# Kernel optimization log

Measured on AMD Instinct MI355X. Metric: run time of the kernel, lower is better.

Reference implementation:

```python
import jax, jax.numpy as jnp
import numpy as np

B, N, EMB = 64, 2048, 128
K1 = 3
L = EMB - K1 + 1            # 126, width after conv1/conv2
K2 = L // 2 + 1             # 64, conv3 kernel width -> conv3 out width = K2 - 1 = 63


def _conv_relu(x, w, b):
    # x: [M, 1, H, W]; w: [O, 1, kh, kw]; VALID conv + bias + relu
    y = jax.lax.conv_general_dilated(
        x, w, window_strides=(1, 1), padding='VALID',
        dimension_numbers=('NCHW', 'OIHW', 'NCHW'))
    return jax.nn.relu(y + b[None, :, None, None])


def _score(pairs, W1, b1, W2, b2, W3, b3, fw1, fb1, fw2, fb2, fw3, fb3):
    # pairs: [M, 2, D] -> score [M]
    x = pairs[:, None]                                  # [M,1,2,D]
    c1 = _conv_relu(x, W1, b1)                          # [M,1,2,L]
    c2 = _conv_relu(x, W2, b2)                          # [M,1,1,L]
    c = jnp.concatenate([c1, c2], axis=2)               # [M,1,3,L]
    c3 = _conv_relu(c, W3, b3)                          # [M,1,1,K2-1]
    h = c3.reshape(c3.shape[0], -1)                     # [M,K2-1]
    h = h @ fw1.T + fb1                                 # [M,K2//4]
    h = h @ fw2.T + fb2                                 # [M,16]
    h = h @ fw3.T + fb3                                 # [M,1]
    return h[:, 0]


def setup_inputs() -> dict:
    key = jax.random.key(0)
    ks = jax.random.split(key, 12)
    users = jax.random.normal(ks[0], (B, N, EMB), jnp.float32)
    top_user = jax.random.normal(ks[1], (B, EMB), jnp.float32)
    question = jax.random.normal(ks[2], (B, EMB), jnp.float32)
    # ragged valid-lengths: uids nonzero for first `len` entries, zero after
    lengths = jax.random.randint(ks[3], (B,), 1, N + 1)
    vals = jax.random.randint(ks[4], (B, N), 1, 10000)
    uids = jnp.where(jnp.arange(N)[None, :] < lengths[:, None], vals, 0).astype(jnp.int64)
    s = 0.1
    return {
        'users': users, 'top_user': top_user, 'question': question, 'uids': uids,
        'W1': jax.random.normal(ks[5], (1, 1, 1, K1), jnp.float32) * s,
        'b1': jnp.zeros((1,), jnp.float32),
        'W2': jax.random.normal(ks[6], (1, 1, 2, K1), jnp.float32) * s,
        'b2': jnp.zeros((1,), jnp.float32),
        'W3': jax.random.normal(ks[7], (1, 1, 3, K2), jnp.float32) * s,
        'b3': jnp.zeros((1,), jnp.float32),
        'fw1': jax.random.normal(ks[8], (K2 // 4, K2 - 1), jnp.float32) * s,
        'fb1': jnp.zeros((K2 // 4,), jnp.float32),
        'fw2': jax.random.normal(ks[9], (16, K2 // 4), jnp.float32) * s,
        'fb2': jnp.zeros((16,), jnp.float32),
        'fw3': jax.random.normal(ks[10], (1, 16), jnp.float32) * s,
        'fb3': jnp.zeros((1,), jnp.float32),
    }


def reference(users, top_user, question, uids,
              W1, b1, W2, b2, W3, b3, fw1, fb1, fw2, fb2, fw3, fb3):
    b, n, d = users.shape
    params = (W1, b1, W2, b2, W3, b3, fw1, fb1, fw2, fb2, fw3, fb3)
    # low-rank pairs: (candidate user, question) for every candidate slot
    q = jnp.broadcast_to(question[:, None], (b, n, d))
    low = jnp.stack([users, q], axis=2).reshape(b * n, 2, d)      # [B*N,2,D]
    high = jnp.stack([top_user, question], axis=1)                # [B,2,D]
    low_s = _score(low, *params).reshape(b, n)                    # [B,N]
    high_s = _score(high, *params)                                # [B]
    # ragged length = index of first zero uid (torch loop breaks there)
    is_zero = uids == 0
    cnt = jnp.where(jnp.any(is_zero, axis=1), jnp.argmax(is_zero, axis=1), n)
    mask = (jnp.arange(n)[None, :] < cnt[:, None]).astype(low_s.dtype)
    return jnp.sum(jax.nn.sigmoid(low_s - high_s[:, None]) * mask)
```

## Files before the change

### kernel.cpp

```cpp
#include <hip/hip_runtime.h>
#include <hip/hip_bf16.h>

typedef __attribute__((ext_vector_type(8))) short short8v;
typedef __attribute__((ext_vector_type(4))) float float4v;

#define NB 64
#define NN 2048
#define ED 128
#define GRID_P 512

#define WS_WEFF  0
#define WS_BEFF  64
#define WS_SHIGH 128
#define WS_QTERM 192
#define WS_QPRE  (192+4096)
#define WS_BPACK (192+4096+8192)
#define WS_QCNT  (WS_BPACK+8192)

static __device__ __forceinline__ unsigned int packbf2(float a, float b) {
    __hip_bfloat162 h = __float22bfloat162_rn(make_float2(a, b));
    return *(unsigned int*)&h;
}

__global__ __launch_bounds__(64) void k_prep(
    const float* __restrict__ top_user, const float* __restrict__ question,
    const float* __restrict__ W1, const float* __restrict__ b1,
    const float* __restrict__ W2, const float* __restrict__ b2,
    const float* __restrict__ W3, const float* __restrict__ b3,
    const float* __restrict__ fw1, const float* __restrict__ fb1,
    const float* __restrict__ fw2, const float* __restrict__ fb2,
    const float* __restrict__ fw3, const float* __restrict__ fb3,
    const int* __restrict__ uids,
    float* __restrict__ ws, float* __restrict__ out)
{
    const int lane = threadIdx.x;
    const int blk = blockIdx.x;

    int act = 0;
    if (blk < NB && lane < 32) act = (uids[blk*NN + lane*64] != 0) ? 1 : 0;

    __shared__ float g[16];
    __shared__ float w3s[192];
    w3s[lane] = W3[lane];
    w3s[64 + lane] = W3[64 + lane];
    w3s[128 + lane] = W3[128 + lane];
    if (lane < 16) {
        float s = 0.f;
        #pragma unroll
        for (int i = 0; i < 16; ++i) s += fw3[i] * fw2[i*16 + lane];
        g[lane] = s;
    }
    __syncthreads();

    if (blk >= NB) {
        const int kt = blk - NB;
        if (kt == 0) {
            if (lane == 0) out[0] = 0.f;
            float wv = 0.f;
            if (lane < 63) {
                #pragma unroll
                for (int k = 0; k < 16; ++k) wv += g[k] * fw1[k*63 + lane];
            }
            ws[WS_WEFF + lane] = wv;
            if (lane == 0) {
                float be = fb3[0];
                #pragma unroll
                for (int i = 0; i < 16; ++i) be += fw3[i] * fb2[i];
                #pragma unroll
                for (int k = 0; k < 16; ++k) be += g[k] * fb1[k];
                ws[WS_BEFF] = be;
            }
        }
        __hip_bfloat16* bp = (__hip_bfloat16*)(ws + WS_BPACK);
        const int g8 = (lane >> 4) * 8, li = lane & 15;
        #pragma unroll
        for (int nt = 0; nt < 4; ++nt) {
            const int tt = nt*16 + li;
            #pragma unroll
            for (int idx = 0; idx < 8; ++idx) {
                const int k = kt*32 + g8 + idx;
                const int j = k - tt;
                const int k2 = k - 128, j2 = k2 - tt;
                const bool v0 = (tt < 63) && (k < 126) && (j >= 0) && (j < 64);
                const bool v2 = (tt < 63) && (k2 >= 0) && (k2 < 126) && (j2 >= 0) && (j2 < 64);
                float v = (v0 ? w3s[j & 63] : 0.f) + (v2 ? w3s[128 + (j2 & 63)] : 0.f);
                bp[((kt*4 + nt)*64 + lane)*8 + idx] = __float2bfloat16(v);
            }
        }
        return;
    }

    {
        const unsigned long long bm = __ballot(act);
        if (lane == 0) ((int*)(ws + WS_QCNT))[blk] = (int)__popcll(bm);
    }

    float wv = 0.f;
    if (lane < 63) {
        #pragma unroll
        for (int k = 0; k < 16; ++k) wv += g[k] * fw1[k*63 + lane];
    }
    float be = fb3[0];
    #pragma unroll
    for (int i = 0; i < 16; ++i) be += fw3[i] * fb2[i];
    #pragma unroll
    for (int k = 0; k < 16; ++k) be += g[k] * fb1[k];

    __shared__ float q[132], tu[132], c1q[128], qt[64];
    __shared__ float4 D4[64];
    const int b = blk;
    ((float2*)q)[lane]  = ((const float2*)(question + b*ED))[lane];
    ((float2*)tu)[lane] = ((const float2*)(top_user + b*ED))[lane];
    if (lane == 63) {
        q[128]=0.f; q[129]=0.f; q[130]=0.f; q[131]=0.f;
        tu[128]=0.f; tu[129]=0.f; tu[130]=0.f; tu[131]=0.f;
    }
    __syncthreads();
    const float w10=W1[0], w11=W1[1], w12=W1[2];
    const float w20=W2[0], w21=W2[1], w22=W2[2];
    const float w23=W2[3], w24=W2[4], w25=W2[5];
    const float b1v=b1[0], b2v=b2[0], b3v=b3[0];
    const int i = 2*lane;
    float c1qa = fmaxf(b1v + w10*q[i]   + w11*q[i+1] + w12*q[i+2], 0.f);
    float c1qb = fmaxf(b1v + w10*q[i+1] + w11*q[i+2] + w12*q[i+3], 0.f);
    float qpa  = w23*q[i]   + w24*q[i+1] + w25*q[i+2];
    float qpb  = w23*q[i+1] + w24*q[i+2] + w25*q[i+3];
    float c1ta = fmaxf(b1v + w10*tu[i]   + w11*tu[i+1] + w12*tu[i+2], 0.f);
    float c1tb = fmaxf(b1v + w10*tu[i+1] + w11*tu[i+2] + w12*tu[i+3], 0.f);
    float c2a  = fmaxf(b2v + w20*tu[i]   + w21*tu[i+1] + w22*tu[i+2] + qpa, 0.f);
    float c2b  = fmaxf(b2v + w20*tu[i+1] + w21*tu[i+2] + w22*tu[i+3] + qpb, 0.f);
    if (lane == 63) { c1qa=0.f; c1qb=0.f; qpa=0.f; qpb=0.f; c1ta=0.f; c1tb=0.f; c2a=0.f; c2b=0.f; }
    c1q[i] = c1qa; c1q[i+1] = c1qb;
    ws[WS_QPRE + b*128 + i]     = qpa;
    ws[WS_QPRE + b*128 + i + 1] = qpb;
    D4[lane] = make_float4(c1ta, c2a, c1tb, c2b);
    __syncthreads();
    float qtv = 0.f;
    if (lane < 63) {
        #pragma unroll
        for (int j = 0; j < 64; ++j) qtv += w3s[64 + j] * c1q[lane + j];
    }
    qt[lane] = qtv;
    ws[WS_QTERM + b*64 + lane] = qtv + b3v;
    __syncthreads();
    float acc0 = b3v + qt[lane];
    float acc1 = 0.f;
    const float2* D2 = (const float2*)D4;
    #pragma unroll
    for (int j = 0; j < 64; ++j) {
        const float2 d = D2[lane + j];
        acc0 = fmaf(w3s[j],       d.x, acc0);
        acc1 = fmaf(w3s[128 + j], d.y, acc1);
    }
    float v = wv * fmaxf(acc0 + acc1, 0.f);
    #pragma unroll
    for (int off = 32; off > 0; off >>= 1) v += __shfl_xor(v, off, 64);
    if (lane == 0) ws[WS_SHIGH + b] = v + be;
}

__global__ __launch_bounds__(256) void k_pairs(
    const float* __restrict__ users, const int* __restrict__ uids,
    float* __restrict__ ws, float* __restrict__ out,
    const float* __restrict__ W1, const float* __restrict__ b1,
    const float* __restrict__ W2, const float* __restrict__ b2)
{
    __shared__ __align__(16) unsigned int X2[2][64][132];
    __shared__ float pscore[2][2][64];
    const int tid = threadIdx.x;
    const int w = tid >> 6, lane = tid & 63;
    const int bid = blockIdx.x;

    const int gfr = lane >> 4, li = lane & 15;
    const int nhalf = w >> 1;
    const int mbase = (w & 1) * 32;
    const int h = lane >> 5, j = lane & 31;
    const int r0 = w * 16;

    const int* qcnti = (const int*)(ws + WS_QCNT);
    const int mycnt = qcnti[lane];
    int incl = mycnt;
    #pragma unroll
    for (int off = 1; off < 64; off <<= 1) {
        const int t = __shfl_up(incl, off, 64);
        if (lane >= off) incl += t;
    }
    const int total = __shfl(incl, 63, 64);

    int cb[4], cidx[4];
    #pragma unroll
    for (int k = 0; k < 4; ++k) {
        const int vid = bid + k*GRID_P;
        if (vid < total) {
            const unsigned long long mm = __ballot(incl <= vid);
            const int bb = (int)__popcll(mm);
            const int prefb = (bb > 0) ? __shfl(incl, bb - 1, 64) : 0;
            cb[k] = bb;
            cidx[k] = vid - prefb;
        } else {
            cb[k] = -1; cidx[k] = 0;
        }
    }
    const int b0 = cb[0], b1i = cb[1], b2i = cb[2], b3i = cb[3];
    if (b0 < 0) return;

    const int pa0 = b0*NN + cidx[0]*64;
    const int pa1 = (b1i >= 0) ? b1i*NN + cidx[1]*64 : 0;
    const int pa2 = (b2i >= 0) ? b2i*NN + cidx[2]*64 : 0;
    const int pa3 = (b3i >= 0) ? b3i*NN + cidx[3]*64 : 0;

    float4 bufA[8], bufB[8];
    #pragma unroll
    for (int pass = 0; pass < 8; ++pass) {
        const int r = r0 + pass*2 + h;
        bufA[pass] = *(const float4*)(users + (size_t)(pa0 + r)*ED + 4*j);
    }
    if (b1i >= 0) {
        #pragma unroll
        for (int pass = 0; pass < 8; ++pass) {
            const int r = r0 + pass*2 + h;
            bufB[pass] = *(const float4*)(users + (size_t)(pa1 + r)*ED + 4*j);
        }
    }

    const __hip_bfloat16* bp = (const __hip_bfloat16*)(ws + WS_BPACK);
    short8v bfr0[8], bfr1[8];
    #pragma unroll
    for (int kt = 0; kt < 8; ++kt) {
        bfr0[kt] = *(const short8v*)(bp + (((kt*4 + nhalf*2 + 0)*64 + lane) << 3));
        bfr1[kt] = *(const short8v*)(bp + (((kt*4 + nhalf*2 + 1)*64 + lane) << 3));
    }

    const int t0 = nhalf*32 + li, t1 = t0 + 16;
    const float wf0 = ws[WS_WEFF + t0], wf1 = ws[WS_WEFF + t1];
    const float beff = ws[WS_BEFF];

    const float qta0 = ws[WS_QTERM + b0*64 + t0], qtb0 = ws[WS_QTERM + b0*64 + t1];
    const float sh0 = ws[WS_SHIGH + b0];
    const float4 qp0 = *(const float4*)&ws[WS_QPRE + b0*128 + 4*j];
    const int m0 = (w == 0) ? uids[pa0 + lane] : 1;

    const int b1c = (b1i >= 0) ? b1i : 0;
    const float qta1 = ws[WS_QTERM + b1c*64 + t0], qtb1 = ws[WS_QTERM + b1c*64 + t1];
    const float sh1 = ws[WS_SHIGH + b1c];
    const float4 qp1 = *(const float4*)&ws[WS_QPRE + b1c*128 + 4*j];
    const int m1 = (w == 0 && b1i >= 0) ? uids[pa1 + lane] : 1;

    const int b2c = (b2i >= 0) ? b2i : 0;
    const float qta2 = ws[WS_QTERM + b2c*64 + t0], qtb2 = ws[WS_QTERM + b2c*64 + t1];
    const float sh2 = ws[WS_SHIGH + b2c];
    const float4 qp2 = *(const float4*)&ws[WS_QPRE + b2c*128 + 4*j];
    const int m2 = (w == 0 && b2i >= 0) ? uids[pa2 + lane] : 1;

    const int b3c = (b3i >= 0) ? b3i : 0;
    const float qta3 = ws[WS_QTERM + b3c*64 + t0], qtb3 = ws[WS_QTERM + b3c*64 + t1];
    const float sh3 = ws[WS_SHIGH + b3c];
    const float4 qp3 = *(const float4*)&ws[WS_QPRE + b3c*128 + 4*j];
    const int m3 = (w == 0 && b3i >= 0) ? uids[pa3 + lane] : 1;

    const float w10=W1[0], w11=W1[1], w12=W1[2];
    const float w20=W2[0], w21=W2[1], w22=W2[2];
    const float b1v=b1[0], b2v=b2[0];

#define PREP_BODY(BUF, XB, QP)                                                      \
    {                                                                               \
        _Pragma("unroll")                                                           \
        for (int pass = 0; pass < 8; ++pass) {                                      \
            const int r = r0 + pass*2 + h;                                          \
            const float4 uu = BUF[pass];                                            \
            const float nx = __shfl(uu.x, (lane + 1) & 63, 64);                     \
            const float ny = __shfl(uu.y, (lane + 1) & 63, 64);                     \
            float c10 = fmaxf(b1v + w10*uu.x + w11*uu.y + w12*uu.z, 0.f);           \
            float c11 = fmaxf(b1v + w10*uu.y + w11*uu.z + w12*uu.w, 0.f);           \
            float c12 = fmaxf(b1v + w10*uu.z + w11*uu.w + w12*nx  , 0.f);           \
            float c13 = fmaxf(b1v + w10*uu.w + w11*nx   + w12*ny  , 0.f);           \
            float c20 = fmaxf(b2v + w20*uu.x + w21*uu.y + w22*uu.z + QP.x, 0.f);    \
            float c21 = fmaxf(b2v + w20*uu.y + w21*uu.z + w22*uu.w + QP.y, 0.f);    \
            float c22 = fmaxf(b2v + w20*uu.z + w21*uu.w + w22*nx   + QP.z, 0.f);    \
            float c23 = fmaxf(b2v + w20*uu.w + w21*nx   + w22*ny   + QP.w, 0.f);    \
            if (j == 31) { c12 = 0.f; c13 = 0.f; c22 = 0.f; c23 = 0.f; }            \
            uint2 v1; v1.x = packbf2(c10, c11); v1.y = packbf2(c12, c13);           \
            uint2 v2; v2.x = packbf2(c20, c21); v2.y = packbf2(c22, c23);           \
            *(uint2*)&X2[XB][r][2*j]      = v1;                                     \
            *(uint2*)&X2[XB][r][64 + 2*j] = v2;                                     \
        }                                                                           \
    }

#define LOAD_INTO(BUF, PA)                                                          \
    {                                                                               \
        _Pragma("unroll")                                                           \
        for (int pass = 0; pass < 8; ++pass) {                                      \
            const int r = r0 + pass*2 + h;                                          \
            BUF[pass] = *(const float4*)(users + (size_t)((PA) + r)*ED + 4*j);      \
        }                                                                           \
    }

    auto gemm = [&](int xb, int psl, float qta, float qtb) {
        float4v acc00 = {0.f,0.f,0.f,0.f}, acc01 = {0.f,0.f,0.f,0.f};
        float4v acc10 = {0.f,0.f,0.f,0.f}, acc11 = {0.f,0.f,0.f,0.f};
        const char* Xb = (const char*)&X2[xb][0][0];
        #pragma unroll
        for (int kt = 0; kt < 8; ++kt) {
            const short8v aa0 = *(const short8v*)(Xb + (mbase + li)*528      + kt*64 + gfr*16);
            const short8v aa1 = *(const short8v*)(Xb + (mbase + 16 + li)*528 + kt*64 + gfr*16);
            acc00 = __builtin_amdgcn_mfma_f32_16x16x32_bf16(aa0, bfr0[kt], acc00, 0, 0, 0);
            acc01 = __builtin_amdgcn_mfma_f32_16x16x32_bf16(aa0, bfr1[kt], acc01, 0, 0, 0);
            acc10 = __builtin_amdgcn_mfma_f32_16x16x32_bf16(aa1, bfr0[kt], acc10, 0, 0, 0);
            acc11 = __builtin_amdgcn_mfma_f32_16x16x32_bf16(aa1, bfr1[kt], acc11, 0, 0, 0);
        }
        #pragma unroll
        for (int mi = 0; mi < 2; ++mi) {
            #pragma unroll
            for (int reg = 0; reg < 4; ++reg) {
                const float a0v = mi ? acc10[reg] : acc00[reg];
                const float a1v = mi ? acc11[reg] : acc01[reg];
                float v = wf0 * fmaxf(a0v + qta, 0.f) + wf1 * fmaxf(a1v + qtb, 0.f);
                v += __shfl_xor(v, 1, 64);
                v += __shfl_xor(v, 2, 64);
                v += __shfl_xor(v, 4, 64);
                v += __shfl_xor(v, 8, 64);
                if (li == 0) pscore[psl][nhalf][mbase + mi*16 + gfr*4 + reg] = v;
            }
        }
    };

    float val = 0.f;
    auto sig = [&](int psl, int m, float sh) {
        if (w == 0) {
            const float d = pscore[psl][0][lane] + pscore[psl][1][lane] + beff - sh;
            if (m != 0) val += 1.f / (1.f + __expf(-d));
        }
    };

    PREP_BODY(bufA, 0, qp0)
    __syncthreads();

    if (b2i >= 0) LOAD_INTO(bufA, pa2)
    gemm(0, 0, qta0, qtb0);
    if (b1i >= 0) PREP_BODY(bufB, 1, qp1)
    __syncthreads();

    sig(0, m0, sh0);
    if (b1i >= 0) {
        if (b3i >= 0) LOAD_INTO(bufB, pa3)
        gemm(1, 1, qta1, qtb1);
        if (b2i >= 0) PREP_BODY(bufA, 0, qp2)
        __syncthreads();

        sig(1, m1, sh1);
        if (b2i >= 0) {
            gemm(0, 0, qta2, qtb2);
            if (b3i >= 0) PREP_BODY(bufB, 1, qp3)
            __syncthreads();

            sig(0, m2, sh2);
            if (b3i >= 0) {
                gemm(1, 1, qta3, qtb3);
                __syncthreads();
                sig(1, m3, sh3);
            }
        }
    }

    if (w == 0) {
        #pragma unroll
        for (int off = 32; off > 0; off >>= 1) val += __shfl_xor(val, off, 64);
        if (lane == 0) atomicAdd(out, val);
    }
#undef PREP_BODY
#undef LOAD_INTO
}

extern "C" void kernel_launch(void* const* d_in, const int* in_sizes, int n_in,
                              void* d_out, int out_size, void* d_ws, size_t ws_size,
                              hipStream_t stream)
{
    const float* users    = (const float*)d_in[0];
    const float* top_user = (const float*)d_in[1];
    const float* question = (const float*)d_in[2];
    const int*   uids     = (const int*)d_in[3];
    const float* W1  = (const float*)d_in[4];
    const float* b1  = (const float*)d_in[5];
    const float* W2  = (const float*)d_in[6];
    const float* b2  = (const float*)d_in[7];
    const float* W3  = (const float*)d_in[8];
    const float* b3  = (const float*)d_in[9];
    const float* fw1 = (const float*)d_in[10];
    const float* fb1 = (const float*)d_in[11];
    const float* fw2 = (const float*)d_in[12];
    const float* fb2 = (const float*)d_in[13];
    const float* fw3 = (const float*)d_in[14];
    const float* fb3 = (const float*)d_in[15];
    float* ws  = (float*)d_ws;
    float* out = (float*)d_out;

    hipLaunchKernelGGL(k_prep, dim3(NB + 8), dim3(64), 0, stream,
                       top_user, question, W1, b1, W2, b2, W3, b3,
                       fw1, fb1, fw2, fb2, fw3, fb3, uids, ws, out);
    hipLaunchKernelGGL(k_pairs, dim3(GRID_P), dim3(256), 0, stream,
                       users, uids, ws, out, W1, b1, W2, b2);
}
```

Baseline: 28.43 us.

## Fuse prep and pair kernels into one launch with atomic bitmask flags

Merges the prep kernel and the pair-scoring kernel into a single persistent launch. The first 72 blocks do the prep work in their first wave and set bits in global bitmasks with release atomics. All blocks spin on those masks before reading the shared workspace, and the users tile and uids are prefetched before the second wait to overlap latency. This removes the second kernel launch and the gap between kernels, but adds a memset call, spin-wait cost, and a reliance on every prep block being co-resident.

```diff
diff --git a/kernel.cpp b/kernel.cpp
--- a/kernel.cpp
+++ b/kernel.cpp
@@ -16,13 +16,15 @@
 #define WS_QPRE  (192+4096)
 #define WS_BPACK (192+4096+8192)
 #define WS_QCNT  (WS_BPACK+8192)
+#define WS_SYNC  (WS_QCNT+64)
 
 static __device__ __forceinline__ unsigned int packbf2(float a, float b) {
     __hip_bfloat162 h = __float22bfloat162_rn(make_float2(a, b));
     return *(unsigned int*)&h;
 }
 
-__global__ __launch_bounds__(64) void k_prep(
+__global__ __launch_bounds__(256) void k_all(
+    const float* __restrict__ users, const int* __restrict__ uids,
     const float* __restrict__ top_user, const float* __restrict__ question,
     const float* __restrict__ W1, const float* __restrict__ b1,
     const float* __restrict__ W2, const float* __restrict__ b2,
@@ -30,145 +32,156 @@
     const float* __restrict__ fw1, const float* __restrict__ fb1,
     const float* __restrict__ fw2, const float* __restrict__ fb2,
     const float* __restrict__ fw3, const float* __restrict__ fb3,
-    const int* __restrict__ uids,
     float* __restrict__ ws, float* __restrict__ out)
 {
-    const int lane = threadIdx.x;
-    const int blk = blockIdx.x;
-
-    int act = 0;
-    if (blk < NB && lane < 32) act = (uids[blk*NN + lane*64] != 0) ? 1 : 0;
-
-    __shared__ float g[16];
-    __shared__ float w3s[192];
-    w3s[lane] = W3[lane];
-    w3s[64 + lane] = W3[64 + lane];
-    w3s[128 + lane] = W3[128 + lane];
-    if (lane < 16) {
-        float s = 0.f;
-        #pragma unroll
-        for (int i = 0; i < 16; ++i) s += fw3[i] * fw2[i*16 + lane];
-        g[lane] = s;
-    }
-    __syncthreads();
-
-    if (blk >= NB) {
-        const int kt = blk - NB;
-        if (kt == 0) {
-            if (lane == 0) out[0] = 0.f;
+    __shared__ __align__(16) unsigned int X2[2][64][132];
+    __shared__ float pscore[2][2][64];
+    __shared__ float q[132], tu[132], c1q[128], qt[64];
+    __shared__ float w3s[192], g[16];
+    __shared__ float4 D4[64];
+
+    const int tid = threadIdx.x;
+    const int w = tid >> 6, lane = tid & 63;
+    const int bid = blockIdx.x;
+
+    unsigned long long* mQC = (unsigned long long*)(ws + WS_SYNC);
+    unsigned long long* mPR = mQC + 1;
+    unsigned long long* mBP = mQC + 2;
+
+    const float w10=W1[0], w11=W1[1], w12=W1[2];
+    const float w20=W2[0], w21=W2[1], w22=W2[2];
+    const float w23=W2[3], w24=W2[4], w25=W2[5];
+    const float b1v=b1[0], b2v=b2[0], b3v=b3[0];
+
+    if (bid < NB) {
+        const int b = bid;
+        if (w == 0) {
+            const int act = (lane < 32) ? ((uids[b*NN + lane*64] != 0) ? 1 : 0) : 0;
+            const unsigned long long bm = __ballot(act);
+            if (lane == 0) {
+                ((int*)(ws + WS_QCNT))[b] = (int)__popcll(bm);
+                __hip_atomic_fetch_or(mQC, 1ull << b, __ATOMIC_RELEASE, __HIP_MEMORY_SCOPE_AGENT);
+            }
+            w3s[lane] = W3[lane]; w3s[64+lane] = W3[64+lane]; w3s[128+lane] = W3[128+lane];
+            if (lane < 16) {
+                float s = 0.f;
+                #pragma unroll
+                for (int i = 0; i < 16; ++i) s += fw3[i] * fw2[i*16 + lane];
+                g[lane] = s;
+            }
+            ((float2*)q)[lane]  = ((const float2*)(question + b*ED))[lane];
+            ((float2*)tu)[lane] = ((const float2*)(top_user + b*ED))[lane];
+            if (lane == 63) {
+                q[128]=0.f; q[129]=0.f; q[130]=0.f; q[131]=0.f;
+                tu[128]=0.f; tu[129]=0.f; tu[130]=0.f; tu[131]=0.f;
+            }
+        }
+        __syncthreads();
+        if (w == 0) {
+            const int i = 2*lane;
+            float c1qa = fmaxf(b1v + w10*q[i]   + w11*q[i+1] + w12*q[i+2], 0.f);
+            float c1qb = fmaxf(b1v + w10*q[i+1] + w11*q[i+2] + w12*q[i+3], 0.f);
+            float qpa  = w23*q[i]   + w24*q[i+1] + w25*q[i+2];
+            float qpb  = w23*q[i+1] + w24*q[i+2] + w25*q[i+3];
+            float c1ta = fmaxf(b1v + w10*tu[i]   + w11*tu[i+1] + w12*tu[i+2], 0.f);
+            float c1tb = fmaxf(b1v + w10*tu[i+1] + w11*tu[i+2] + w12*tu[i+3], 0.f);
+            float c2a  = fmaxf(b2v + w20*tu[i]   + w21*tu[i+1] + w22*tu[i+2] + qpa, 0.f);
+            float c2b  = fmaxf(b2v + w20*tu[i+1] + w21*tu[i+2] + w22*tu[i+3] + qpb, 0.f);
+            if (lane == 63) { c1qa=0.f; c1qb=0.f; qpa=0.f; qpb=0.f; c1ta=0.f; c1tb=0.f; c2a=0.f; c2b=0.f; }
+            c1q[i] = c1qa; c1q[i+1] = c1qb;
+            ws[WS_QPRE + b*128 + i]     = qpa;
+            ws[WS_QPRE + b*128 + i + 1] = qpb;
+            D4[lane] = make_float4(c1ta, c2a, c1tb, c2b);
+        }
+        __syncthreads();
+        if (w == 0) {
+            float qtv = 0.f;
+            if (lane < 63) {
+                #pragma unroll
+                for (int jj = 0; jj < 64; ++jj) qtv += w3s[64 + jj] * c1q[lane + jj];
+            }
+            qt[lane] = qtv;
+            ws[WS_QTERM + b*64 + lane] = qtv + b3v;
+        }
+        __syncthreads();
+        if (w == 0) {
             float wv = 0.f;
             if (lane < 63) {
                 #pragma unroll
                 for (int k = 0; k < 16; ++k) wv += g[k] * fw1[k*63 + lane];
             }
-            ws[WS_WEFF + lane] = wv;
+            float be = fb3[0];
+            #pragma unroll
+            for (int i = 0; i < 16; ++i) be += fw3[i] * fb2[i];
+            #pragma unroll
+            for (int k = 0; k < 16; ++k) be += g[k] * fb1[k];
+            float acc0 = b3v + qt[lane];
+            float acc1 = 0.f;
+            const float2* D2 = (const float2*)D4;
+            #pragma unroll
+            for (int jj = 0; jj < 64; ++jj) {
+                const float2 d = D2[lane + jj];
+                acc0 = fmaf(w3s[jj],       d.x, acc0);
+                acc1 = fmaf(w3s[128 + jj], d.y, acc1);
+            }
+            float v = wv * fmaxf(acc0 + acc1, 0.f);
+            #pragma unroll
+            for (int off = 32; off > 0; off >>= 1) v += __shfl_xor(v, off, 64);
             if (lane == 0) {
-                float be = fb3[0];
+                ws[WS_SHIGH + b] = v + be;
+                __hip_atomic_fetch_or(mPR, 1ull << b, __ATOMIC_RELEASE, __HIP_MEMORY_SCOPE_AGENT);
+            }
+        }
+    } else if (bid < NB + 8) {
+        const int kt = bid - NB;
+        if (w == 0) {
+            w3s[lane] = W3[lane]; w3s[64+lane] = W3[64+lane]; w3s[128+lane] = W3[128+lane];
+            if (lane < 16) {
+                float s = 0.f;
                 #pragma unroll
-                for (int i = 0; i < 16; ++i) be += fw3[i] * fb2[i];
+                for (int i = 0; i < 16; ++i) s += fw3[i] * fw2[i*16 + lane];
+                g[lane] = s;
+            }
+        }
+        __syncthreads();
+        if (w == 0) {
+            if (kt == 0) {
+                if (lane == 0) out[0] = 0.f;
+                float wv = 0.f;
+                if (lane < 63) {
+                    #pragma unroll
+                    for (int k = 0; k < 16; ++k) wv += g[k] * fw1[k*63 + lane];
+                }
+                ws[WS_WEFF + lane] = wv;
+                if (lane == 0) {
+                    float be = fb3[0];
+                    #pragma unroll
+                    for (int i = 0; i < 16; ++i) be += fw3[i] * fb2[i];
+                    #pragma unroll
+                    for (int k = 0; k < 16; ++k) be += g[k] * fb1[k];
+                    ws[WS_BEFF] = be;
+                }
+            }
+            __hip_bfloat16* bp = (__hip_bfloat16*)(ws + WS_BPACK);
+            const int g8 = (lane >> 4) * 8, li2 = lane & 15;
+            #pragma unroll
+            for (int nt = 0; nt < 4; ++nt) {
+                const int tt = nt*16 + li2;
                 #pragma unroll
-                for (int k = 0; k < 16; ++k) be += g[k] * fb1[k];
-                ws[WS_BEFF] = be;
-            }
-        }
-        __hip_bfloat16* bp = (__hip_bfloat16*)(ws + WS_BPACK);
-        const int g8 = (lane >> 4) * 8, li = lane & 15;
-        #pragma unroll
-        for (int nt = 0; nt < 4; ++nt) {
-            const int tt = nt*16 + li;
-            #pragma unroll
-            for (int idx = 0; idx < 8; ++idx) {
-                const int k = kt*32 + g8 + idx;
-                const int j = k - tt;
-                const int k2 = k - 128, j2 = k2 - tt;
-                const bool v0 = (tt < 63) && (k < 126) && (j >= 0) && (j < 64);
-                const bool v2 = (tt < 63) && (k2 >= 0) && (k2 < 126) && (j2 >= 0) && (j2 < 64);
-                float v = (v0 ? w3s[j & 63] : 0.f) + (v2 ? w3s[128 + (j2 & 63)] : 0.f);
-                bp[((kt*4 + nt)*64 + lane)*8 + idx] = __float2bfloat16(v);
-            }
-        }
-        return;
-    }
-
-    {
-        const unsigned long long bm = __ballot(act);
-        if (lane == 0) ((int*)(ws + WS_QCNT))[blk] = (int)__popcll(bm);
-    }
-
-    float wv = 0.f;
-    if (lane < 63) {
-        #pragma unroll
-        for (int k = 0; k < 16; ++k) wv += g[k] * fw1[k*63 + lane];
-    }
-    float be = fb3[0];
-    #pragma unroll
-    for (int i = 0; i < 16; ++i) be += fw3[i] * fb2[i];
-    #pragma unroll
-    for (int k = 0; k < 16; ++k) be += g[k] * fb1[k];
-
-    __shared__ float q[132], tu[132], c1q[128], qt[64];
-    __shared__ float4 D4[64];
-    const int b = blk;
-    ((float2*)q)[lane]  = ((const float2*)(question + b*ED))[lane];
-    ((float2*)tu)[lane] = ((const float2*)(top_user + b*ED))[lane];
-    if (lane == 63) {
-        q[128]=0.f; q[129]=0.f; q[130]=0.f; q[131]=0.f;
-        tu[128]=0.f; tu[129]=0.f; tu[130]=0.f; tu[131]=0.f;
-    }
-    __syncthreads();
-    const float w10=W1[0], w11=W1[1], w12=W1[2];
-    const float w20=W2[0], w21=W2[1], w22=W2[2];
-    const float w23=W2[3], w24=W2[4], w25=W2[5];
-    const float b1v=b1[0], b2v=b2[0], b3v=b3[0];
-    const int i = 2*lane;
-    float c1qa = fmaxf(b1v + w10*q[i]   + w11*q[i+1] + w12*q[i+2], 0.f);
-    float c1qb = fmaxf(b1v + w10*q[i+1] + w11*q[i+2] + w12*q[i+3], 0.f);
-    float qpa  = w23*q[i]   + w24*q[i+1] + w25*q[i+2];
-    float qpb  = w23*q[i+1] + w24*q[i+2] + w25*q[i+3];
-    float c1ta = fmaxf(b1v + w10*tu[i]   + w11*tu[i+1] + w12*tu[i+2], 0.f);
-    float c1tb = fmaxf(b1v + w10*tu[i+1] + w11*tu[i+2] + w12*tu[i+3], 0.f);
-    float c2a  = fmaxf(b2v + w20*tu[i]   + w21*tu[i+1] + w22*tu[i+2] + qpa, 0.f);
-    float c2b  = fmaxf(b2v + w20*tu[i+1] + w21*tu[i+2] + w22*tu[i+3] + qpb, 0.f);
-    if (lane == 63) { c1qa=0.f; c1qb=0.f; qpa=0.f; qpb=0.f; c1ta=0.f; c1tb=0.f; c2a=0.f; c2b=0.f; }
-    c1q[i] = c1qa; c1q[i+1] = c1qb;
-    ws[WS_QPRE + b*128 + i]     = qpa;
-    ws[WS_QPRE + b*128 + i + 1] = qpb;
-    D4[lane] = make_float4(c1ta, c2a, c1tb, c2b);
-    __syncthreads();
-    float qtv = 0.f;
-    if (lane < 63) {
-        #pragma unroll
-        for (int j = 0; j < 64; ++j) qtv += w3s[64 + j] * c1q[lane + j];
-    }
-    qt[lane] = qtv;
-    ws[WS_QTERM + b*64 + lane] = qtv + b3v;
-    __syncthreads();
-    float acc0 = b3v + qt[lane];
-    float acc1 = 0.f;
-    const float2* D2 = (const float2*)D4;
-    #pragma unroll
-    for (int j = 0; j < 64; ++j) {
-        const float2 d = D2[lane + j];
-        acc0 = fmaf(w3s[j],       d.x, acc0);
-        acc1 = fmaf(w3s[128 + j], d.y, acc1);
-    }
-    float v = wv * fmaxf(acc0 + acc1, 0.f);
-    #pragma unroll
-    for (int off = 32; off > 0; off >>= 1) v += __shfl_xor(v, off, 64);
-    if (lane == 0) ws[WS_SHIGH + b] = v + be;
-}
-
-__global__ __launch_bounds__(256) void k_pairs(
-    const float* __restrict__ users, const int* __restrict__ uids,
-    float* __restrict__ ws, float* __restrict__ out,
-    const float* __restrict__ W1, const float* __restrict__ b1,
-    const float* __restrict__ W2, const float* __restrict__ b2)
-{
-    __shared__ __align__(16) unsigned int X2[2][64][132];
-    __shared__ float pscore[2][2][64];
-    const int tid = threadIdx.x;
-    const int w = tid >> 6, lane = tid & 63;
-    const int bid = blockIdx.x;
+                for (int idx = 0; idx < 8; ++idx) {
+                    const int k = kt*32 + g8 + idx;
+                    const int jj = k - tt;
+                    const int k2 = k - 128, j2 = k2 - tt;
+                    const bool v0 = (tt < 63) && (k < 126) && (jj >= 0) && (jj < 64);
+                    const bool v2 = (tt < 63) && (k2 >= 0) && (k2 < 126) && (j2 >= 0) && (j2 < 64);
+                    float v = (v0 ? w3s[jj & 63] : 0.f) + (v2 ? w3s[128 + (j2 & 63)] : 0.f);
+                    bp[((kt*4 + nt)*64 + lane)*8 + idx] = __float2bfloat16(v);
+                }
+            }
+            if (lane == 0)
+                __hip_atomic_fetch_or(mBP, 1ull << kt, __ATOMIC_RELEASE, __HIP_MEMORY_SCOPE_AGENT);
+        }
+    }
 
     const int gfr = lane >> 4, li = lane & 15;
     const int nhalf = w >> 1;
@@ -176,8 +189,14 @@
     const int h = lane >> 5, j = lane & 31;
     const int r0 = w * 16;
 
-    const int* qcnti = (const int*)(ws + WS_QCNT);
-    const int mycnt = qcnti[lane];
+    if (tid == 0) {
+        while (__hip_atomic_load(mQC, __ATOMIC_RELAXED, __HIP_MEMORY_SCOPE_AGENT) != ~0ull)
+            __builtin_amdgcn_s_sleep(1);
+        (void)__hip_atomic_load(mQC, __ATOMIC_ACQUIRE, __HIP_MEMORY_SCOPE_AGENT);
+    }
+    __syncthreads();
+
+    const int mycnt = ((const int*)(ws + WS_QCNT))[lane];
     int incl = mycnt;
     #pragma unroll
     for (int off = 1; off < 64; off <<= 1) {
@@ -194,11 +213,8 @@
             const unsigned long long mm = __ballot(incl <= vid);
             const int bb = (int)__popcll(mm);
             const int prefb = (bb > 0) ? __shfl(incl, bb - 1, 64) : 0;
-            cb[k] = bb;
-            cidx[k] = vid - prefb;
-        } else {
-            cb[k] = -1; cidx[k] = 0;
-        }
+            cb[k] = bb; cidx[k] = vid - prefb;
+        } else { cb[k] = -1; cidx[k] = 0; }
     }
     const int b0 = cb[0], b1i = cb[1], b2i = cb[2], b3i = cb[3];
     if (b0 < 0) return;
@@ -221,6 +237,18 @@
             bufB[pass] = *(const float4*)(users + (size_t)(pa1 + r)*ED + 4*j);
         }
     }
+    const int m0 = (w == 0) ? uids[pa0 + lane] : 1;
+    const int m1 = (w == 0 && b1i >= 0) ? uids[pa1 + lane] : 1;
+    const int m2 = (w == 0 && b2i >= 0) ? uids[pa2 + lane] : 1;
+    const int m3 = (w == 0 && b3i >= 0) ? uids[pa3 + lane] : 1;
+
+    if (tid == 0) {
+        while (__hip_atomic_load(mPR, __ATOMIC_RELAXED, __HIP_MEMORY_SCOPE_AGENT) != ~0ull ||
+               __hip_atomic_load(mBP, __ATOMIC_RELAXED, __HIP_MEMORY_SCOPE_AGENT) != 0xFFull)
+            __builtin_amdgcn_s_sleep(1);
+        (void)__hip_atomic_load(mPR, __ATOMIC_ACQUIRE, __HIP_MEMORY_SCOPE_AGENT);
+    }
+    __syncthreads();
 
     const __hip_bfloat16* bp = (const __hip_bfloat16*)(ws + WS_BPACK);
     short8v bfr0[8], bfr1[8];
@@ -229,7 +257,6 @@
         bfr0[kt] = *(const short8v*)(bp + (((kt*4 + nhalf*2 + 0)*64 + lane) << 3));
         bfr1[kt] = *(const short8v*)(bp + (((kt*4 + nhalf*2 + 1)*64 + lane) << 3));
     }
-
     const int t0 = nhalf*32 + li, t1 = t0 + 16;
     const float wf0 = ws[WS_WEFF + t0], wf1 = ws[WS_WEFF + t1];
     const float beff = ws[WS_BEFF];
@@ -237,29 +264,18 @@
     const float qta0 = ws[WS_QTERM + b0*64 + t0], qtb0 = ws[WS_QTERM + b0*64 + t1];
     const float sh0 = ws[WS_SHIGH + b0];
     const float4 qp0 = *(const float4*)&ws[WS_QPRE + b0*128 + 4*j];
-    const int m0 = (w == 0) ? uids[pa0 + lane] : 1;
-
     const int b1c = (b1i >= 0) ? b1i : 0;
     const float qta1 = ws[WS_QTERM + b1c*64 + t0], qtb1 = ws[WS_QTERM + b1c*64 + t1];
     const float sh1 = ws[WS_SHIGH + b1c];
     const float4 qp1 = *(const float4*)&ws[WS_QPRE + b1c*128 + 4*j];
-    const int m1 = (w == 0 && b1i >= 0) ? uids[pa1 + lane] : 1;
-
     const int b2c = (b2i >= 0) ? b2i : 0;
     const float qta2 = ws[WS_QTERM + b2c*64 + t0], qtb2 = ws[WS_QTERM + b2c*64 + t1];
     const float sh2 = ws[WS_SHIGH + b2c];
     const float4 qp2 = *(const float4*)&ws[WS_QPRE + b2c*128 + 4*j];
-    const int m2 = (w == 0 && b2i >= 0) ? uids[pa2 + lane] : 1;
-
     const int b3c = (b3i >= 0) ? b3i : 0;
     const float qta3 = ws[WS_QTERM + b3c*64 + t0], qtb3 = ws[WS_QTERM + b3c*64 + t1];
     const float sh3 = ws[WS_SHIGH + b3c];
     const float4 qp3 = *(const float4*)&ws[WS_QPRE + b3c*128 + 4*j];
-    const int m3 = (w == 0 && b3i >= 0) ? uids[pa3 + lane] : 1;
-
-    const float w10=W1[0], w11=W1[1], w12=W1[2];
-    const float w20=W2[0], w21=W2[1], w22=W2[2];
-    const float b1v=b1[0], b2v=b2[0];
 
 #define PREP_BODY(BUF, XB, QP)                                                      \
     {                                                                               \
@@ -393,9 +409,9 @@
     float* ws  = (float*)d_ws;
     float* out = (float*)d_out;
 
-    hipLaunchKernelGGL(k_prep, dim3(NB + 8), dim3(64), 0, stream,
-                       top_user, question, W1, b1, W2, b2, W3, b3,
-                       fw1, fb1, fw2, fb2, fw3, fb3, uids, ws, out);
-    hipLaunchKernelGGL(k_pairs, dim3(GRID_P), dim3(256), 0, stream,
-                       users, uids, ws, out, W1, b1, W2, b2);
+    hipMemsetAsync((char*)ws + (size_t)WS_SYNC * 4, 0, 24, stream);
+    hipLaunchKernelGGL(k_all, dim3(GRID_P), dim3(256), 0, stream,
+                       users, uids, top_user, question,
+                       W1, b1, W2, b2, W3, b3,
+                       fw1, fb1, fw2, fb2, fw3, fb3, ws, out);
 }
```

After: 46.53 us. 63.7% more time.

## Double grid size, process two tiles per block with a single LDS buffer

Applied to the files above, without the earlier changes.

The grid of the pair-scoring kernel doubles, so each block handles at most two 64-row tiles of valid candidates instead of four. The LDS staging drops from two buffers to one, and the prefetch-overlapped four-stage pipeline becomes a simple sequential prep/gemm/sig sequence for each tile. Blocks with no work now exit early, before loading anything. The aim is more parallelism across CUs and lower LDS use for better occupancy, at the cost of losing the overlap between global loads, prep and MFMA work inside a block.

```diff
diff --git a/kernel.cpp b/kernel.cpp
--- a/kernel.cpp
+++ b/kernel.cpp
@@ -7,7 +7,7 @@
 #define NB 64
 #define NN 2048
 #define ED 128
-#define GRID_P 512
+#define GRID_P 1024
 
 #define WS_WEFF  0
 #define WS_BEFF  64
@@ -164,11 +164,37 @@
     const float* __restrict__ W1, const float* __restrict__ b1,
     const float* __restrict__ W2, const float* __restrict__ b2)
 {
-    __shared__ __align__(16) unsigned int X2[2][64][132];
+    __shared__ __align__(16) unsigned int X[64][132];
     __shared__ float pscore[2][2][64];
     const int tid = threadIdx.x;
     const int w = tid >> 6, lane = tid & 63;
     const int bid = blockIdx.x;
+
+    const int* qcnti = (const int*)(ws + WS_QCNT);
+    int incl = qcnti[lane];
+    #pragma unroll
+    for (int off = 1; off < 64; off <<= 1) {
+        const int t = __shfl_up(incl, off, 64);
+        if (lane >= off) incl += t;
+    }
+    const int total = __shfl(incl, 63, 64);
+    if (bid >= total) return;
+
+    int cb[2], cidx[2];
+    #pragma unroll
+    for (int k = 0; k < 2; ++k) {
+        const int vid = bid + k*GRID_P;
+        if (vid < total) {
+            const unsigned long long mm = __ballot(incl <= vid);
+            const int bb = (int)__popcll(mm);
+            const int prefb = (bb > 0) ? __shfl(incl, bb - 1, 64) : 0;
+            cb[k] = bb; cidx[k] = vid - prefb;
+        } else { cb[k] = -1; cidx[k] = 0; }
+    }
+    const int b0 = cb[0], b1i = cb[1];
+    const bool has1 = (b1i >= 0);
+    const int pa0 = b0*NN + cidx[0]*64;
+    const int pa1 = has1 ? b1i*NN + cidx[1]*64 : 0;
 
     const int gfr = lane >> 4, li = lane & 15;
     const int nhalf = w >> 1;
@@ -176,51 +202,21 @@
     const int h = lane >> 5, j = lane & 31;
     const int r0 = w * 16;
 
-    const int* qcnti = (const int*)(ws + WS_QCNT);
-    const int mycnt = qcnti[lane];
-    int incl = mycnt;
-    #pragma unroll
-    for (int off = 1; off < 64; off <<= 1) {
-        const int t = __shfl_up(incl, off, 64);
-        if (lane >= off) incl += t;
-    }
-    const int total = __shfl(incl, 63, 64);
-
-    int cb[4], cidx[4];
-    #pragma unroll
-    for (int k = 0; k < 4; ++k) {
-        const int vid = bid + k*GRID_P;
-        if (vid < total) {
-            const unsigned long long mm = __ballot(incl <= vid);
-            const int bb = (int)__popcll(mm);
-            const int prefb = (bb > 0) ? __shfl(incl, bb - 1, 64) : 0;
-            cb[k] = bb;
-            cidx[k] = vid - prefb;
-        } else {
-            cb[k] = -1; cidx[k] = 0;
-        }
-    }
-    const int b0 = cb[0], b1i = cb[1], b2i = cb[2], b3i = cb[3];
-    if (b0 < 0) return;
-
-    const int pa0 = b0*NN + cidx[0]*64;
-    const int pa1 = (b1i >= 0) ? b1i*NN + cidx[1]*64 : 0;
-    const int pa2 = (b2i >= 0) ? b2i*NN + cidx[2]*64 : 0;
-    const int pa3 = (b3i >= 0) ? b3i*NN + cidx[3]*64 : 0;
-
     float4 bufA[8], bufB[8];
     #pragma unroll
     for (int pass = 0; pass < 8; ++pass) {
         const int r = r0 + pass*2 + h;
         bufA[pass] = *(const float4*)(users + (size_t)(pa0 + r)*ED + 4*j);
     }
-    if (b1i >= 0) {
+    if (has1) {
         #pragma unroll
         for (int pass = 0; pass < 8; ++pass) {
             const int r = r0 + pass*2 + h;
             bufB[pass] = *(const float4*)(users + (size_t)(pa1 + r)*ED + 4*j);
         }
     }
+    const int m0 = (w == 0) ? uids[pa0 + lane] : 1;
+    const int m1 = (w == 0 && has1) ? uids[pa1 + lane] : 1;
 
     const __hip_bfloat16* bp = (const __hip_bfloat16*)(ws + WS_BPACK);
     short8v bfr0[8], bfr1[8];
@@ -233,35 +229,19 @@
     const int t0 = nhalf*32 + li, t1 = t0 + 16;
     const float wf0 = ws[WS_WEFF + t0], wf1 = ws[WS_WEFF + t1];
     const float beff = ws[WS_BEFF];
-
     const float qta0 = ws[WS_QTERM + b0*64 + t0], qtb0 = ws[WS_QTERM + b0*64 + t1];
     const float sh0 = ws[WS_SHIGH + b0];
     const float4 qp0 = *(const float4*)&ws[WS_QPRE + b0*128 + 4*j];
-    const int m0 = (w == 0) ? uids[pa0 + lane] : 1;
-
-    const int b1c = (b1i >= 0) ? b1i : 0;
+    const int b1c = has1 ? b1i : 0;
     const float qta1 = ws[WS_QTERM + b1c*64 + t0], qtb1 = ws[WS_QTERM + b1c*64 + t1];
     const float sh1 = ws[WS_SHIGH + b1c];
     const float4 qp1 = *(const float4*)&ws[WS_QPRE + b1c*128 + 4*j];
-    const int m1 = (w == 0 && b1i >= 0) ? uids[pa1 + lane] : 1;
-
-    const int b2c = (b2i >= 0) ? b2i : 0;
-    const float qta2 = ws[WS_QTERM + b2c*64 + t0], qtb2 = ws[WS_QTERM + b2c*64 + t1];
-    const float sh2 = ws[WS_SHIGH + b2c];
-    const float4 qp2 = *(const float4*)&ws[WS_QPRE + b2c*128 + 4*j];
-    const int m2 = (w == 0 && b2i >= 0) ? uids[pa2 + lane] : 1;
-
-    const int b3c = (b3i >= 0) ? b3i : 0;
-    const float qta3 = ws[WS_QTERM + b3c*64 + t0], qtb3 = ws[WS_QTERM + b3c*64 + t1];
-    const float sh3 = ws[WS_SHIGH + b3c];
-    const float4 qp3 = *(const float4*)&ws[WS_QPRE + b3c*128 + 4*j];
-    const int m3 = (w == 0 && b3i >= 0) ? uids[pa3 + lane] : 1;
 
     const float w10=W1[0], w11=W1[1], w12=W1[2];
     const float w20=W2[0], w21=W2[1], w22=W2[2];
     const float b1v=b1[0], b2v=b2[0];
 
-#define PREP_BODY(BUF, XB, QP)                                                      \
+#define PREP_BODY(BUF, QP)                                                          \
     {                                                                               \
         _Pragma("unroll")                                                           \
         for (int pass = 0; pass < 8; ++pass) {                                      \
@@ -280,24 +260,15 @@
             if (j == 31) { c12 = 0.f; c13 = 0.f; c22 = 0.f; c23 = 0.f; }            \
             uint2 v1; v1.x = packbf2(c10, c11); v1.y = packbf2(c12, c13);           \
             uint2 v2; v2.x = packbf2(c20, c21); v2.y = packbf2(c22, c23);           \
-            *(uint2*)&X2[XB][r][2*j]      = v1;                                     \
-            *(uint2*)&X2[XB][r][64 + 2*j] = v2;                                     \
+            *(uint2*)&X[r][2*j]      = v1;                                          \
+            *(uint2*)&X[r][64 + 2*j] = v2;                                          \
         }                                                                           \
     }
 
-#define LOAD_INTO(BUF, PA)                                                          \
-    {                                                                               \
-        _Pragma("unroll")                                                           \
-        for (int pass = 0; pass < 8; ++pass) {                                      \
-            const int r = r0 + pass*2 + h;                                          \
-            BUF[pass] = *(const float4*)(users + (size_t)((PA) + r)*ED + 4*j);      \
-        }                                                                           \
-    }
-
-    auto gemm = [&](int xb, int psl, float qta, float qtb) {
+    auto gemm = [&](int psl, float qta, float qtb) {
         float4v acc00 = {0.f,0.f,0.f,0.f}, acc01 = {0.f,0.f,0.f,0.f};
         float4v acc10 = {0.f,0.f,0.f,0.f}, acc11 = {0.f,0.f,0.f,0.f};
-        const char* Xb = (const char*)&X2[xb][0][0];
+        const char* Xb = (const char*)&X[0][0];
         #pragma unroll
         for (int kt = 0; kt < 8; ++kt) {
             const short8v aa0 = *(const short8v*)(Xb + (mbase + li)*528      + kt*64 + gfr*16);
@@ -331,34 +302,18 @@
         }
     };
 
-    PREP_BODY(bufA, 0, qp0)
-    __syncthreads();
-
-    if (b2i >= 0) LOAD_INTO(bufA, pa2)
-    gemm(0, 0, qta0, qtb0);
-    if (b1i >= 0) PREP_BODY(bufB, 1, qp1)
+    PREP_BODY(bufA, qp0)
+    __syncthreads();
+    gemm(0, qta0, qtb0);
     __syncthreads();
 
     sig(0, m0, sh0);
-    if (b1i >= 0) {
-        if (b3i >= 0) LOAD_INTO(bufB, pa3)
-        gemm(1, 1, qta1, qtb1);
-        if (b2i >= 0) PREP_BODY(bufA, 0, qp2)
+    if (has1) {
+        PREP_BODY(bufB, qp1)
         __syncthreads();
-
+        gemm(1, qta1, qtb1);
+        __syncthreads();
         sig(1, m1, sh1);
-        if (b2i >= 0) {
-            gemm(0, 0, qta2, qtb2);
-            if (b3i >= 0) PREP_BODY(bufB, 1, qp3)
-            __syncthreads();
-
-            sig(0, m2, sh2);
-            if (b3i >= 0) {
-                gemm(1, 1, qta3, qtb3);
-                __syncthreads();
-                sig(1, m3, sh3);
-            }
-        }
     }
 
     if (w == 0) {
@@ -367,7 +322,6 @@
         if (lane == 0) atomicAdd(out, val);
     }
 #undef PREP_BODY
-#undef LOAD_INTO
 }
 
 extern "C" void kernel_launch(void* const* d_in, const int* in_sizes, int n_in,
```

Result: slower. 30.98 us (+9.0%).
